# Performance work log

Hardware: AMD Instinct MI355X
Metric: run time of the kernel (lower is better)

## Reference

```python
import jax, jax.numpy as jnp
import numpy as np

N_NODES = 100000
N_EDGES = 1600000
N_HIDDEN = 128
EPS = 1e-12  # matches torch F.normalize default eps


def setup_inputs() -> dict:
    key = jax.random.key(0)
    k1, k2, k3, k4 = jax.random.split(key, 4)
    emb = jax.random.normal(k1, (N_NODES, N_HIDDEN), dtype=jnp.float32)
    src = jax.random.randint(k2, (N_EDGES,), 0, N_NODES, dtype=jnp.int64)
    dst = jax.random.randint(k3, (N_EDGES,), 0, N_NODES, dtype=jnp.int64)
    d = jnp.ones((N_HIDDEN,), dtype=jnp.float32)
    scale = jax.random.uniform(k4, (1,), dtype=jnp.float32)
    return {"emb": emb, "src": src, "dst": dst, "d": d, "scale": scale}


def reference(emb, src, dst, d, scale):
    # L2 normalize rows (torch F.normalize p=2, dim=1, eps=1e-12)
    norm = jnp.linalg.norm(emb, axis=1, keepdims=True)
    e = emb / jnp.maximum(norm, EPS)          # [N, H]
    ew = e * d                                 # diag scale, [N, H]
    # edge-wise u_dot_v: dot(ew[src], e[dst]) -> [E, 1]
    z = jnp.sum(ew[src] * e[dst], axis=-1, keepdims=True)
    return z * scale
```

## Files before the change

kernel.cpp:

```cpp
#include <hip/hip_runtime.h>

#define H 128
#define EPS 1e-12f

static __device__ __forceinline__ float bf_lo(unsigned int v) {
    return __uint_as_float(v << 16);
}
static __device__ __forceinline__ float bf_hi(unsigned int v) {
    return __uint_as_float(v & 0xFFFF0000u);
}
static __device__ __forceinline__ unsigned int f2bf_rne(float f) {
    unsigned int u = __float_as_uint(f);
    return (u + 0x7FFFu + ((u >> 16) & 1u)) >> 16;
}

static __device__ __forceinline__ float dot8(uint4 a, uint4 b,
                                             float4 d0, float4 d1, float p) {
    p = fmaf(bf_lo(a.x) * d0.x, bf_lo(b.x), p);
    p = fmaf(bf_hi(a.x) * d0.y, bf_hi(b.x), p);
    p = fmaf(bf_lo(a.y) * d0.z, bf_lo(b.y), p);
    p = fmaf(bf_hi(a.y) * d0.w, bf_hi(b.y), p);
    p = fmaf(bf_lo(a.z) * d1.x, bf_lo(b.z), p);
    p = fmaf(bf_hi(a.z) * d1.y, bf_hi(b.z), p);
    p = fmaf(bf_lo(a.w) * d1.z, bf_lo(b.w), p);
    p = fmaf(bf_hi(a.w) * d1.w, bf_hi(b.w), p);
    return p;
}

__global__ void norm_quant_kernel(const float* __restrict__ emb,
                                  unsigned int* __restrict__ pool,
                                  int n_nodes) {
    int row = blockIdx.x * (blockDim.x >> 6) + (threadIdx.x >> 6);
    if (row >= n_nodes) return;
    int lane = threadIdx.x & 63;
    const float* p = emb + (size_t)row * H + lane * 2;
    float vx = __builtin_nontemporal_load(p);
    float vy = __builtin_nontemporal_load(p + 1);
    float ss = vx * vx + vy * vy;
#pragma unroll
    for (int off = 32; off; off >>= 1) ss += __shfl_xor(ss, off);
    float inv = 1.0f / fmaxf(sqrtf(ss), EPS);
    unsigned int ua = f2bf_rne(vx * inv);
    unsigned int ub = f2bf_rne(vy * inv);
    pool[(size_t)row * 64 + lane] = ua | (ub << 16);
}

__global__ void edge_dot_bf16_kernel(const uint4* __restrict__ pool,
                                     const int* __restrict__ src,
                                     const int* __restrict__ dst,
                                     const float* __restrict__ d,
                                     const float* __restrict__ scale,
                                     float* __restrict__ out,
                                     int n_edges) {
    int lane = threadIdx.x & 63;
    int sub  = lane >> 3;
    int q    = lane & 7;

    float4 dv0 = ((const float4*)d)[q * 4 + 0];
    float4 dv1 = ((const float4*)d)[q * 4 + 1];
    float4 dv2 = ((const float4*)d)[q * 4 + 2];
    float4 dv3 = ((const float4*)d)[q * 4 + 3];
    float sc = scale[0];

    int waveId = (blockIdx.x * blockDim.x + threadIdx.x) >> 6;
    int nWaves = (gridDim.x * blockDim.x) >> 6;
    int last = n_edges - 1;

    for (int ebase = waveId * 16; ebase < n_edges; ebase += nWaves * 16) {
        int e0 = ebase + sub;
        int e1 = ebase + 8 + sub;
        bool w0 = (e0 < n_edges);
        bool w1 = (e1 < n_edges);
        int c0 = w0 ? e0 : last;
        int c1 = w1 ? e1 : last;

        int s0 = __builtin_nontemporal_load(src + c0);
        int t0 = __builtin_nontemporal_load(dst + c0);
        int s1 = __builtin_nontemporal_load(src + c1);
        int t1 = __builtin_nontemporal_load(dst + c1);

        const uint4* pa0 = pool + (size_t)s0 * 16 + q * 2;
        const uint4* pb0 = pool + (size_t)t0 * 16 + q * 2;
        const uint4* pa1 = pool + (size_t)s1 * 16 + q * 2;
        const uint4* pb1 = pool + (size_t)t1 * 16 + q * 2;
        uint4 a00 = pa0[0];
        uint4 a01 = pa0[1];
        uint4 b00 = pb0[0];
        uint4 b01 = pb0[1];
        uint4 a10 = pa1[0];
        uint4 a11 = pa1[1];
        uint4 b10 = pb1[0];
        uint4 b11 = pb1[1];

        float p0 = dot8(a00, b00, dv0, dv1, 0.0f);
        p0 = dot8(a01, b01, dv2, dv3, p0);
        float p1 = dot8(a10, b10, dv0, dv1, 0.0f);
        p1 = dot8(a11, b11, dv2, dv3, p1);

        p0 += __shfl_xor(p0, 1);
        p1 += __shfl_xor(p1, 1);
        p0 += __shfl_xor(p0, 2);
        p1 += __shfl_xor(p1, 2);
        p0 += __shfl_xor(p0, 4);
        p1 += __shfl_xor(p1, 4);

        if (q == 0) {
            if (w0) __builtin_nontemporal_store(p0 * sc, out + e0);
            if (w1) __builtin_nontemporal_store(p1 * sc, out + e1);
        }
    }
}


__global__ void inv_norm_kernel(const float* __restrict__ emb,
                                float* __restrict__ inv,
                                int n_nodes) {
    int row = blockIdx.x * (blockDim.x >> 6) + (threadIdx.x >> 6);
    if (row >= n_nodes) return;
    int lane = threadIdx.x & 63;
    const float2* p = (const float2*)(emb + (size_t)row * H);
    float2 v = p[lane];
    float ss = v.x * v.x + v.y * v.y;
#pragma unroll
    for (int off = 32; off; off >>= 1) ss += __shfl_xor(ss, off);
    if (lane == 0) inv[row] = 1.0f / fmaxf(sqrtf(ss), EPS);
}

__global__ void edge_dot_kernel(const float* __restrict__ emb,
                                const float* __restrict__ inv,
                                const int* __restrict__ src,
                                const int* __restrict__ dst,
                                const float* __restrict__ d,
                                const float* __restrict__ scale,
                                float* __restrict__ out,
                                int n_edges) {
    int edge = blockIdx.x * (blockDim.x >> 6) + (threadIdx.x >> 6);
    if (edge >= n_edges) return;
    int lane = threadIdx.x & 63;
    int s = src[edge];
    int t = dst[edge];
    const float2* ps = (const float2*)(emb + (size_t)s * H);
    const float2* pt = (const float2*)(emb + (size_t)t * H);
    float2 dv = ((const float2*)d)[lane];
    float2 a = ps[lane];
    float2 b = pt[lane];
    float p = a.x * dv.x * b.x + a.y * dv.y * b.y;
#pragma unroll
    for (int off = 32; off; off >>= 1) p += __shfl_xor(p, off);
    if (lane == 0) out[edge] = p * inv[s] * inv[t] * scale[0];
}

extern "C" void kernel_launch(void* const* d_in, const int* in_sizes, int n_in,
                              void* d_out, int out_size, void* d_ws, size_t ws_size,
                              hipStream_t stream) {
    const float* emb   = (const float*)d_in[0];
    const int*   src   = (const int*)d_in[1];
    const int*   dst   = (const int*)d_in[2];
    const float* d     = (const float*)d_in[3];
    const float* scale = (const float*)d_in[4];
    float* out = (float*)d_out;

    int n_nodes = in_sizes[0] / H;
    int n_edges = in_sizes[1];

    size_t pool_bytes = (size_t)n_nodes * H * 2;

    if (ws_size >= pool_bytes) {
        unsigned int* pool = (unsigned int*)d_ws;

        int blocks1 = (n_nodes + 3) / 4;
        norm_quant_kernel<<<blocks1, 256, 0, stream>>>(emb, pool, n_nodes);

        int blocks2 = 2048;
        edge_dot_bf16_kernel<<<blocks2, 256, 0, stream>>>(
            (const uint4*)pool, src, dst, d, scale, out, n_edges);
    } else {
        float* inv = (float*)d_ws;
        int blocks1 = (n_nodes + 3) / 4;
        inv_norm_kernel<<<blocks1, 256, 0, stream>>>(emb, inv, n_nodes);
        int blocks2 = (n_edges + 3) / 4;
        edge_dot_kernel<<<blocks2, 256, 0, stream>>>(emb, inv, src, dst, d,
                                                     scale, out, n_edges);
    }
}
```

Measured before the change: 125.7 us.

## Split edge dot into per-slice feature passes with partial-sum combine kernel

Replaces the single edge kernel with a kernel where each block handles one of eight 16-feature slices of the bf16 node pool for all edges, writing per-slice partial dots to a workspace buffer. A second kernel sums the eight partials and applies the scale. The likely intent is to shrink the working set each block touches, giving better cache locality for the random gathers, and to drop the cross-lane shuffles. In exchange, src/dst indices are read eight times and about 51 MB of partials are written and read back, and the path only runs when the workspace is large enough.

```diff
diff --git a/kernel.cpp b/kernel.cpp
--- a/kernel.cpp
+++ b/kernel.cpp
@@ -44,6 +44,58 @@
     unsigned int ub = f2bf_rne(vy * inv);
     pool[(size_t)row * 64 + lane] = ua | (ub << 16);
 }
+
+__global__ void edge_slice_kernel(const uint4* __restrict__ pool,
+                                  const int* __restrict__ src,
+                                  const int* __restrict__ dst,
+                                  const float* __restrict__ d,
+                                  float* __restrict__ part,
+                                  int n_edges) {
+    int slice = blockIdx.x & 7;
+    int g     = blockIdx.x >> 3;
+    int nG    = gridDim.x >> 3;
+
+    const float4* d4 = (const float4*)(d + slice * 16);
+    float4 dv0 = d4[0];
+    float4 dv1 = d4[1];
+    float4 dv2 = d4[2];
+    float4 dv3 = d4[3];
+
+    float* pw = part + (size_t)slice * n_edges;
+    int tid    = g * blockDim.x + threadIdx.x;
+    int stride = nG * blockDim.x;
+
+    for (int e = tid; e < n_edges; e += stride) {
+        int s = __builtin_nontemporal_load(src + e);
+        int t = __builtin_nontemporal_load(dst + e);
+        const uint4* pa = pool + (size_t)s * 16 + slice * 2;
+        const uint4* pb = pool + (size_t)t * 16 + slice * 2;
+        uint4 a0 = pa[0];
+        uint4 a1 = pa[1];
+        uint4 b0 = pb[0];
+        uint4 b1 = pb[1];
+        float p = dot8(a0, b0, dv0, dv1, 0.0f);
+        p = dot8(a1, b1, dv2, dv3, p);
+        __builtin_nontemporal_store(p, pw + e);
+    }
+}
+
+__global__ void combine_kernel(const float* __restrict__ part,
+                               const float* __restrict__ scale,
+                               float* __restrict__ out,
+                               int n_edges) {
+    float sc = scale[0];
+    int tid    = blockIdx.x * blockDim.x + threadIdx.x;
+    int stride = gridDim.x * blockDim.x;
+    for (int e = tid; e < n_edges; e += stride) {
+        float acc = 0.0f;
+#pragma unroll
+        for (int s = 0; s < 8; ++s)
+            acc += __builtin_nontemporal_load(part + (size_t)s * n_edges + e);
+        __builtin_nontemporal_store(acc * sc, out + e);
+    }
+}
+
 
 __global__ void edge_dot_bf16_kernel(const uint4* __restrict__ pool,
                                      const int* __restrict__ src,
@@ -164,15 +216,24 @@
     int n_edges = in_sizes[1];
 
     size_t pool_bytes = (size_t)n_nodes * H * 2;
-
-    if (ws_size >= pool_bytes) {
+    size_t part_bytes = (size_t)8 * n_edges * sizeof(float);
+
+    if (ws_size >= pool_bytes + part_bytes) {
         unsigned int* pool = (unsigned int*)d_ws;
+        float* part = (float*)((char*)d_ws + pool_bytes);
 
         int blocks1 = (n_nodes + 3) / 4;
         norm_quant_kernel<<<blocks1, 256, 0, stream>>>(emb, pool, n_nodes);
 
-        int blocks2 = 2048;
-        edge_dot_bf16_kernel<<<blocks2, 256, 0, stream>>>(
+        edge_slice_kernel<<<2048, 256, 0, stream>>>(
+            (const uint4*)pool, src, dst, d, part, n_edges);
+
+        combine_kernel<<<2048, 256, 0, stream>>>(part, scale, out, n_edges);
+    } else if (ws_size >= pool_bytes) {
+        unsigned int* pool = (unsigned int*)d_ws;
+        int blocks1 = (n_nodes + 3) / 4;
+        norm_quant_kernel<<<blocks1, 256, 0, stream>>>(emb, pool, n_nodes);
+        edge_dot_bf16_kernel<<<2048, 256, 0, stream>>>(
             (const uint4*)pool, src, dst, d, scale, out, n_edges);
     } else {
         float* inv = (float*)d_ws;
```

Result: slower. 368.4 us (+193.1%).
